# Kernel optimization log

Measured on AMD Instinct MI355X. Metric: run time of the kernel, lower is better.

The kernel has to match this reference:

```python
import jax, jax.numpy as jnp
import numpy as np

# Similarity layer (simnets-tf), L2 similarity, ksize=3x3, stride 1, SAME padding,
# no normalization term, out_of_bounds_value = 0.
# sim[b,n,i,j] = -sum_{c,p,q} |w[n,c,p,q]| * (x_patch[b,c,i+p,j+q] - t[n,c,p,q])^2
# Expanded: -conv(x^2, |w|) + 2*conv(x, |w|*t) - sum(|w|*t^2)  (exact since pad value is 0).

B, C, H, W = 16, 64, 112, 112
N, KH, KW = 256, 3, 3
PAD = 1  # SAME padding for ksize 3


def _conv(inp, ker):
    # inp: [B,C,H',W'] padded, ker: [N,C,KH,KW] -> [B,N,H,W], VALID
    return jax.lax.conv_general_dilated(
        inp, ker, window_strides=(1, 1), padding='VALID',
        dimension_numbers=('NCHW', 'OIHW', 'NCHW'))


def setup_inputs() -> dict:
    key = jax.random.key(0)
    k1, k2, k3 = jax.random.split(key, 3)
    x = jax.random.normal(k1, (B, C, H, W), dtype=jnp.float32)
    sweights = jax.random.normal(k2, (N, C, KH, KW), dtype=jnp.float32)
    templates = jax.random.normal(k3, (N, C, KH, KW), dtype=jnp.float32)
    return {'x': x, 'sweights': sweights, 'templates': templates}


def reference(x, sweights, templates):
    w = jnp.abs(sweights)                      # layer applies tf.abs to weights
    xp = jnp.pad(x, ((0, 0), (0, 0), (PAD, PAD), (PAD, PAD)),
                 constant_values=0.0)          # out_of_bounds_value = 0
    sq_term = _conv(xp * xp, w)                # sum w * x^2 -> [B,N,H,W]
    cross = _conv(xp, w * templates)           # sum w * t * x
    const = jnp.sum(w * templates * templates, axis=(1, 2, 3))  # [N]
    return -sq_term + 2.0 * cross - const[None, :, None, None]
```

## Files before the change

### kernel.cpp

```cpp
#include <hip/hip_runtime.h>
#include <stdint.h>

#define B_ 16
#define C_ 64
#define H_ 112
#define W_ 112
#define N_ 256

typedef __attribute__((ext_vector_type(8))) short short8;
typedef __attribute__((ext_vector_type(4))) float floatx4;

__device__ __forceinline__ uint32_t f2bf_bits(float f) {
  uint32_t u = __float_as_uint(f);
  return (u + 0x7fffu + ((u >> 16) & 1u)) >> 16;
}

__global__ __launch_bounds__(256) void xform_x(const float* __restrict__ x,
                                               uint32_t* __restrict__ xq) {
  __shared__ float ls[64][113];
  int bi = blockIdx.x;
  int b = bi / H_, i = bi % H_;
  const float* xbase = x + ((size_t)b * C_) * (H_ * W_) + (size_t)i * W_;
  for (int idx = threadIdx.x; idx < C_ * W_; idx += 256) {
    int c = idx / W_, j = idx - c * W_;
    ls[c][j] = xbase[(size_t)c * (H_ * W_) + j];
  }
  __syncthreads();
  uint32_t* orow = xq + ((size_t)(b * H_ + i)) * (W_ * C_);
  for (int idx = threadIdx.x; idx < W_ * C_; idx += 256) {
    int j = idx >> 6, c = idx & 63;
    float v = ls[c][j];
    float v2 = v * v;
    orow[idx] = f2bf_bits(v) | (f2bf_bits(v2) << 16);
  }
}

__global__ __launch_bounds__(64) void prep_wc(const float* __restrict__ sw,
                                              const float* __restrict__ tp,
                                              uint32_t* __restrict__ Wg,
                                              float* __restrict__ cN) {
  int n = blockIdx.x, c = threadIdx.x;
  int cg = c >> 5, ci = c & 31;
  int kk = ci >> 4, pos = ci & 15;
  const float* swp = sw + (size_t)(n * C_ + c) * 9;
  const float* tpp = tp + (size_t)(n * C_ + c) * 9;
  float s = 0.f;
#pragma unroll
  for (int tap = 0; tap < 9; ++tap) {
    float w = fabsf(swp[tap]);
    float t = tpp[tap];
    s += w * t * t;
    uint32_t v = f2bf_bits(2.0f * w * t) | (f2bf_bits(-w) << 16);
    Wg[(size_t)(((cg * 9 + tap) * 2 + kk) * (N_ * 16)) + n * 16 + pos] = v;
  }
#pragma unroll
  for (int off = 32; off > 0; off >>= 1) s += __shfl_down(s, off);
  if (c == 0) cN[n] = s;
}

__global__ __launch_bounds__(512, 4) void sim_main(const uint32_t* __restrict__ xq,
                                                   const uint32_t* __restrict__ Wg,
                                                   const float* __restrict__ cN,
                                                   float* __restrict__ out) {
  __shared__ uint32_t xs[18 * 18 * 32];

  int bx = blockIdx.x;
  int nb = bx & 1;
  bx >>= 1;
  int b = bx / 49;
  int rem = bx - b * 49;
  int rt = rem / 7, ct = rem - rt * 7;
  int r0 = rt * 16, c0 = ct * 16;
  int tid = threadIdx.x;
  int lane = tid & 63, wv = tid >> 6;
  int wn = wv & 1, wp = wv >> 1;
  int l15 = lane & 15, l4 = lane >> 4;

  floatx4 acc[4][4];
#pragma unroll
  for (int a = 0; a < 4; ++a)
#pragma unroll
    for (int p = 0; p < 4; ++p) acc[a][p] = (floatx4){0.f, 0.f, 0.f, 0.f};

  const uint32_t* xim = xq + (size_t)b * (H_ * W_ * C_);
  const uint32_t* wlane = Wg + (nb * 128 + wn * 64 + l15) * 16 + l4 * 4;

  for (int cg = 0; cg < 2; ++cg) {
    if (cg) __syncthreads();
    for (int idx = tid; idx < 324 * 8; idx += 512) {
      int s = idx >> 3, ch = idx & 7;
      int row = s / 18, col = s - row * 18;
      int gi = r0 - 1 + row, gj = c0 - 1 + col;
      uint4 v = make_uint4(0u, 0u, 0u, 0u);
      if ((unsigned)gi < (unsigned)H_ && (unsigned)gj < (unsigned)W_)
        v = *(const uint4*)(xim + ((size_t)(gi * W_ + gj)) * C_ + cg * 32 + ch * 4);
      *(uint4*)(&xs[s * 32 + ((ch ^ (s & 7)) << 2)]) = v;
    }
    __syncthreads();

#pragma unroll 1
    for (int tap = 0; tap < 9; ++tap) {
      int dp = tap / 3, dq = tap - dp * 3;
      const uint32_t* wp0 = wlane + (size_t)((cg * 9 + tap) * 2) * (N_ * 16);
      int sb[4], sx[4];
#pragma unroll
      for (int pt = 0; pt < 4; ++pt) {
        int s = (wp * 4 + pt + dp) * 18 + l15 + dq;
        sb[pt] = s * 32;
        sx[pt] = s & 7;
      }
#pragma unroll
      for (int kk = 0; kk < 2; ++kk) {
        int chb = kk * 4 + l4;
        short8 af[4], bfr[4];
#pragma unroll
        for (int nt = 0; nt < 4; ++nt)
          af[nt] = *(const short8*)(wp0 + (size_t)kk * (N_ * 16) + nt * 16 * 16);
#pragma unroll
        for (int pt = 0; pt < 4; ++pt)
          bfr[pt] = *(const short8*)(&xs[sb[pt] + ((chb ^ sx[pt]) << 2)]);
#pragma unroll
        for (int nt = 0; nt < 4; ++nt)
#pragma unroll
          for (int pt = 0; pt < 4; ++pt)
            acc[nt][pt] =
                __builtin_amdgcn_mfma_f32_16x16x32_bf16(af[nt], bfr[pt], acc[nt][pt], 0, 0, 0);
      }
    }
  }

#pragma unroll
  for (int nt = 0; nt < 4; ++nt) {
#pragma unroll
    for (int v = 0; v < 4; ++v) {
      int n = nb * 128 + wn * 64 + nt * 16 + l4 * 4 + v;
      float cv = cN[n];
#pragma unroll
      for (int pt = 0; pt < 4; ++pt) {
        int r = r0 + wp * 4 + pt;
        int col = c0 + l15;
        out[(((size_t)b * N_ + n) * H_ + r) * W_ + col] = acc[nt][pt][v] - cv;
      }
    }
  }
}

extern "C" void kernel_launch(void* const* d_in, const int* in_sizes, int n_in,
                              void* d_out, int out_size, void* d_ws, size_t ws_size,
                              hipStream_t stream) {
  const float* x = (const float*)d_in[0];
  const float* sw = (const float*)d_in[1];
  const float* tp = (const float*)d_in[2];
  float* out = (float*)d_out;

  const size_t xq_bytes = (size_t)B_ * H_ * W_ * C_ * 4;
  const size_t wg_bytes = (size_t)2 * 9 * 2 * N_ * 16 * 4;
  uint32_t* xq = (uint32_t*)d_ws;
  uint32_t* Wg = (uint32_t*)((char*)d_ws + xq_bytes);
  float* cN = (float*)((char*)d_ws + xq_bytes + wg_bytes);

  xform_x<<<dim3(B_ * H_), dim3(256), 0, stream>>>(x, xq);
  prep_wc<<<dim3(N_), dim3(64), 0, stream>>>(sw, tp, Wg, cN);
  sim_main<<<dim3(2 * B_ * 7 * 7), dim3(512), 0, stream>>>(xq, Wg, cN, out);
}
```

Baseline: 400.1 us.

## Stage weight fragments through double-buffered LDS with async global-to-LDS loads

Each wave used to fetch its MFMA A-fragments (weights) straight from global memory for every tap, so the four waves sharing a weight slice read the same data repeatedly. Now each block copies its 128-channel weight slice for the next k-step into a double-buffered LDS area using global_load_lds. The tap/kk loops are flattened into one 36-step loop with a barrier per step, and the second channel group of the input tile is restaged halfway through. This cuts redundant global/L1 weight traffic and prefetches one step ahead, but adds 16 KB of LDS per block, which can lower resident blocks per CU, and adds a barrier every step.

```diff
diff --git a/kernel.cpp b/kernel.cpp
--- a/kernel.cpp
+++ b/kernel.cpp
@@ -9,6 +9,9 @@
 
 typedef __attribute__((ext_vector_type(8))) short short8;
 typedef __attribute__((ext_vector_type(4))) float floatx4;
+
+typedef __attribute__((address_space(1))) const uint32_t gas_u32;
+typedef __attribute__((address_space(3))) uint32_t las_u32;
 
 __device__ __forceinline__ uint32_t f2bf_bits(float f) {
   uint32_t u = __float_as_uint(f);
@@ -63,6 +66,7 @@
                                                    const float* __restrict__ cN,
                                                    float* __restrict__ out) {
   __shared__ uint32_t xs[18 * 18 * 32];
+  __shared__ uint32_t ws[2 * 2048];
 
   int bx = blockIdx.x;
   int nb = bx & 1;
@@ -83,10 +87,9 @@
     for (int p = 0; p < 4; ++p) acc[a][p] = (floatx4){0.f, 0.f, 0.f, 0.f};
 
   const uint32_t* xim = xq + (size_t)b * (H_ * W_ * C_);
-  const uint32_t* wlane = Wg + (nb * 128 + wn * 64 + l15) * 16 + l4 * 4;
+  const uint32_t* wslice = Wg + nb * 2048;
 
-  for (int cg = 0; cg < 2; ++cg) {
-    if (cg) __syncthreads();
+  auto stage_xs = [&](int cg) {
     for (int idx = tid; idx < 324 * 8; idx += 512) {
       int s = idx >> 3, ch = idx & 7;
       int row = s / 18, col = s - row * 18;
@@ -96,37 +99,48 @@
         v = *(const uint4*)(xim + ((size_t)(gi * W_ + gj)) * C_ + cg * 32 + ch * 4);
       *(uint4*)(&xs[s * 32 + ((ch ^ (s & 7)) << 2)]) = v;
     }
-    __syncthreads();
+  };
+  auto stage_w = [&](int step) {
+    const uint32_t* g = wslice + (size_t)step * (N_ * 16) + wv * 256 + lane * 4;
+    uint32_t* l = &ws[(step & 1) * 2048 + wv * 256];
+    __builtin_amdgcn_global_load_lds((gas_u32*)g, (las_u32*)l, 16, 0, 0);
+  };
+
+  stage_xs(0);
+  stage_w(0);
+  __syncthreads();
+
+  int awb = (wn * 64 + l15) * 16 + l4 * 4;
 
 #pragma unroll 1
-    for (int tap = 0; tap < 9; ++tap) {
-      int dp = tap / 3, dq = tap - dp * 3;
-      const uint32_t* wp0 = wlane + (size_t)((cg * 9 + tap) * 2) * (N_ * 16);
-      int sb[4], sx[4];
+  for (int s = 0; s < 36; ++s) {
+    if (s < 35) stage_w(s + 1);
+    if (s == 18) {
+      stage_xs(1);
+      __syncthreads();
+    }
+    int t2 = (s < 18) ? s : s - 18;
+    int tap = t2 >> 1, kk = t2 & 1;
+    int dp = tap / 3, dq = tap - dp * 3;
+    int chb = kk * 4 + l4;
+    int buf = s & 1;
+
+    short8 af[4], bfr[4];
 #pragma unroll
-      for (int pt = 0; pt < 4; ++pt) {
-        int s = (wp * 4 + pt + dp) * 18 + l15 + dq;
-        sb[pt] = s * 32;
-        sx[pt] = s & 7;
-      }
+    for (int nt = 0; nt < 4; ++nt)
+      af[nt] = *(const short8*)(&ws[buf * 2048 + awb + nt * 256]);
 #pragma unroll
-      for (int kk = 0; kk < 2; ++kk) {
-        int chb = kk * 4 + l4;
-        short8 af[4], bfr[4];
+    for (int pt = 0; pt < 4; ++pt) {
+      int st = (wp * 4 + pt + dp) * 18 + l15 + dq;
+      bfr[pt] = *(const short8*)(&xs[st * 32 + ((chb ^ (st & 7)) << 2)]);
+    }
 #pragma unroll
-        for (int nt = 0; nt < 4; ++nt)
-          af[nt] = *(const short8*)(wp0 + (size_t)kk * (N_ * 16) + nt * 16 * 16);
+    for (int nt = 0; nt < 4; ++nt)
 #pragma unroll
-        for (int pt = 0; pt < 4; ++pt)
-          bfr[pt] = *(const short8*)(&xs[sb[pt] + ((chb ^ sx[pt]) << 2)]);
-#pragma unroll
-        for (int nt = 0; nt < 4; ++nt)
-#pragma unroll
-          for (int pt = 0; pt < 4; ++pt)
-            acc[nt][pt] =
-                __builtin_amdgcn_mfma_f32_16x16x32_bf16(af[nt], bfr[pt], acc[nt][pt], 0, 0, 0);
-      }
-    }
+      for (int pt = 0; pt < 4; ++pt)
+        acc[nt][pt] =
+            __builtin_amdgcn_mfma_f32_16x16x32_bf16(af[nt], bfr[pt], acc[nt][pt], 0, 0, 0);
+    if (s < 35) __syncthreads();
   }
 
 #pragma unroll
```

After: 380.9 us. 4.8% less time.
